# Performance work log

Measured on AMD Instinct MI355X. Metric: run time of the kernel, lower is better.

The kernel has to match this reference:

```python
import jax, jax.numpy as jnp
import numpy as np

N_NODES = 100_000
N_EDGES = 1_600_000
NEG_SLOPE = 0.2

# layer configs: (in_channels, heads, out_channels, has_proj)
LAYERS = [(193, 8, 16, True), (128, 8, 16, False), (128, 8, 16, False), (128, 8, 8, True)]


def _gat_params(key, fin, H, C):
    ks = jax.random.split(key, 6)
    s = 1.0 / np.sqrt(fin)
    Wl = jax.random.normal(ks[0], (fin, H * C), dtype=jnp.float32) * s
    bl = jax.random.normal(ks[1], (H * C,), dtype=jnp.float32) * 0.01
    Wr = jax.random.normal(ks[2], (fin, H * C), dtype=jnp.float32) * s
    br = jax.random.normal(ks[3], (H * C,), dtype=jnp.float32) * 0.01
    att = jax.random.normal(ks[4], (H, C), dtype=jnp.float32) * (1.0 / np.sqrt(C))
    bias = jax.random.normal(ks[5], (H * C,), dtype=jnp.float32) * 0.01
    return Wl, bl, Wr, br, att, bias


def setup_inputs() -> dict:
    key = jax.random.key(0)
    ks = jax.random.split(key, 16)
    inp = {}
    inp['x'] = jax.random.normal(ks[0], (N_NODES, 193), dtype=jnp.float32)
    inp['edge_index'] = jax.random.randint(ks[1], (2, N_EDGES), 0, N_NODES, dtype=jnp.int64)
    for li, (fin, H, C, _) in enumerate(LAYERS, start=1):
        Wl, bl, Wr, br, att, bias = _gat_params(ks[1 + li], fin, H, C)
        inp[f'Wl{li}'] = Wl; inp[f'bl{li}'] = bl
        inp[f'Wr{li}'] = Wr; inp[f'br{li}'] = br
        inp[f'att{li}'] = att; inp[f'bias{li}'] = bias
    # residual projections where in_channels != heads*out_channels
    inp['proj1_W'] = jax.random.normal(ks[8], (193, 128), dtype=jnp.float32) * (1.0 / np.sqrt(193))
    inp['proj1_b'] = jax.random.normal(ks[9], (128,), dtype=jnp.float32) * 0.01
    inp['proj4_W'] = jax.random.normal(ks[10], (128, 64), dtype=jnp.float32) * (1.0 / np.sqrt(128))
    inp['proj4_b'] = jax.random.normal(ks[11], (64,), dtype=jnp.float32) * 0.01
    inp['lin1_W'] = jax.random.normal(ks[12], (64, 32), dtype=jnp.float32) * (1.0 / np.sqrt(64))
    inp['lin1_b'] = jax.random.normal(ks[13], (32,), dtype=jnp.float32) * 0.01
    return inp


def _gatv2(x, src, dst, Wl, bl, Wr, br, att, bias):
    # x: [N, Fin]; att: [H, C]
    N = x.shape[0]
    H, C = att.shape
    xl = (x @ Wl + bl).reshape(N, H, C)  # source transform
    xr = (x @ Wr + br).reshape(N, H, C)  # destination transform
    m = xl[src] + xr[dst]                # [E, H, C] edge gather
    e = jnp.einsum('ehc,hc->eh', jax.nn.leaky_relu(m, NEG_SLOPE), att)  # [E, H]
    emax = jax.ops.segment_max(e, dst, num_segments=N)  # per-dst softmax max
    p = jnp.exp(e - emax[dst])
    denom = jax.ops.segment_sum(p, dst, num_segments=N)
    alpha = p / (denom[dst] + 1e-16)     # [E, H]
    out = jax.ops.segment_sum(alpha[:, :, None] * xl[src], dst, num_segments=N)  # [N, H, C]
    return out.reshape(N, H * C) + bias


def _forward(x, edge_index, params):
    src, dst = edge_index[0], edge_index[1]
    h = x
    for li in range(4):
        Wl, bl, Wr, br, att, bias, projW, projb = params[li]
        g = _gatv2(h, src, dst, Wl, bl, Wr, br, att, bias)
        res = h @ projW + projb if projW is not None else h
        h = jax.nn.gelu(g + res, approximate=False)
    Wf, bf = params[4]
    return h @ Wf + bf


def reference(x, edge_index,
              Wl1, bl1, Wr1, br1, att1, bias1,
              Wl2, bl2, Wr2, br2, att2, bias2,
              Wl3, bl3, Wr3, br3, att3, bias3,
              Wl4, bl4, Wr4, br4, att4, bias4,
              proj1_W, proj1_b, proj4_W, proj4_b, lin1_W, lin1_b):
    params = [
        (Wl1, bl1, Wr1, br1, att1, bias1, proj1_W, proj1_b),
        (Wl2, bl2, Wr2, br2, att2, bias2, None, None),
        (Wl3, bl3, Wr3, br3, att3, bias3, None, None),
        (Wl4, bl4, Wr4, br4, att4, bias4, proj4_W, proj4_b),
        (lin1_W, lin1_b),
    ]
    return _forward(x, edge_index, params)
```

## Files before the change

kernel.cpp:

```cpp
#include <hip/hip_runtime.h>
#include <hip/hip_bf16.h>

#define NNODES 100000
#define NPR 12500
#define SCAP 262144

typedef short s16x8 __attribute__((ext_vector_type(8)));
typedef float f32x4 __attribute__((ext_vector_type(4)));
typedef unsigned long long u64;

__device__ inline ushort f2bf(float f) {
    uint u = __float_as_uint(f);
    uint r = u + 0x7fffu + ((u >> 16) & 1u);
    return (ushort)(r >> 16);
}
__device__ inline float bf2f(ushort u) { return __uint_as_float(((uint)u) << 16); }
__device__ inline float bflo(uint u) { return __uint_as_float(u << 16); }
__device__ inline float bfhi(uint u) { return __uint_as_float(u & 0xffff0000u); }

__device__ inline void gl_lds16(const ushort* g, ushort* l) {
    __builtin_amdgcn_global_load_lds((const __attribute__((address_space(1))) void*)g,
                                     (__attribute__((address_space(3))) void*)l, 16, 0, 0);
}

__global__ void hist_kernel(const int* __restrict__ dst, int E, int* __restrict__ deg) {
    int e = blockIdx.x * blockDim.x + threadIdx.x;
    if (e < E) atomicAdd(&deg[dst[e]], 1);
}

__global__ __launch_bounds__(256) void scan_part(const int* __restrict__ deg,
                                                 int* __restrict__ bsum, int n) {
    int t = threadIdx.x;
    int base = blockIdx.x * 1024 + t * 4;
    int4 v = make_int4(0, 0, 0, 0);
    if (base + 3 < n) v = *(const int4*)(deg + base);
    else {
        if (base + 0 < n) v.x = deg[base + 0];
        if (base + 1 < n) v.y = deg[base + 1];
        if (base + 2 < n) v.z = deg[base + 2];
    }
    int s = v.x + v.y + v.z + v.w;
#pragma unroll
    for (int o = 1; o < 64; o <<= 1) s += __shfl_xor(s, o);
    __shared__ int ws[4];
    if ((t & 63) == 0) ws[t >> 6] = s;
    __syncthreads();
    if (t == 0) bsum[blockIdx.x] = ws[0] + ws[1] + ws[2] + ws[3];
}

__global__ __launch_bounds__(128) void scan_bsum(int* __restrict__ bsum, int nb,
                                                 int* __restrict__ rowptr, int n) {
    __shared__ int s[128];
    int t = threadIdx.x;
    int v = (t < nb) ? bsum[t] : 0;
    s[t] = v;
    __syncthreads();
#pragma unroll
    for (int o = 1; o < 128; o <<= 1) {
        int u = (t >= o) ? s[t - o] : 0;
        __syncthreads();
        s[t] += u;
        __syncthreads();
    }
    if (t < nb) bsum[t] = s[t] - v;
    if (t == 127) rowptr[n] = s[127];
}

__global__ __launch_bounds__(256) void scan_apply(const int* __restrict__ deg,
                                                  const int* __restrict__ bsum,
                                                  int* __restrict__ rowptr, int n) {
    int t = threadIdx.x;
    int base = blockIdx.x * 1024 + t * 4;
    int4 v = make_int4(0, 0, 0, 0);
    if (base + 3 < n) v = *(const int4*)(deg + base);
    else {
        if (base + 0 < n) v.x = deg[base + 0];
        if (base + 1 < n) v.y = deg[base + 1];
        if (base + 2 < n) v.z = deg[base + 2];
    }
    int s = v.x + v.y + v.z + v.w;
    int lane = t & 63, w = t >> 6;
    int incl = s;
#pragma unroll
    for (int o = 1; o < 64; o <<= 1) {
        int u = __shfl_up(incl, o);
        if (lane >= o) incl += u;
    }
    __shared__ int wsum[4];
    if (lane == 63) wsum[w] = incl;
    __syncthreads();
    int woff = 0;
    if (w > 0) woff += wsum[0];
    if (w > 1) woff += wsum[1];
    if (w > 2) woff += wsum[2];
    int off = bsum[blockIdx.x] + woff + (incl - s);
    int4 r;
    r.x = off;
    r.y = off + v.x;
    r.z = r.y + v.y;
    r.w = r.z + v.z;
    if (base + 3 < n) *(int4*)(rowptr + base) = r;
    else {
        if (base + 0 < n) rowptr[base + 0] = r.x;
        if (base + 1 < n) rowptr[base + 1] = r.y;
        if (base + 2 < n) rowptr[base + 2] = r.z;
    }
}

__global__ __launch_bounds__(256) void bucket_edges(const int* __restrict__ src,
                                                    const int* __restrict__ dst, int E,
                                                    int* __restrict__ rcount,
                                                    u64* __restrict__ stage) {
    __shared__ int cnt[8];
    __shared__ int base[8];
    const int t = threadIdx.x;
    if (t < 8) cnt[t] = 0;
    __syncthreads();
    const int e0 = blockIdx.x * 2048 + t;
    int d[8], s[8], r[8], off[8];
#pragma unroll
    for (int i = 0; i < 8; ++i) {
        int e = e0 + i * 256;
        bool v = e < E;
        int ee = min(e, E - 1);
        d[i] = dst[ee];
        s[i] = src[ee];
        r[i] = d[i] / NPR;
        off[i] = v ? atomicAdd(&cnt[r[i]], 1) : -1;
    }
    __syncthreads();
    if (t < 8) base[t] = atomicAdd(&rcount[t], cnt[t]);
    __syncthreads();
#pragma unroll
    for (int i = 0; i < 8; ++i) {
        if (off[i] >= 0) {
            int slot = base[r[i]] + off[i];
            if (slot < SCAP)
                stage[(size_t)r[i] * SCAP + slot] = ((u64)(uint)d[i] << 32) | (uint)s[i];
        }
    }
}

__global__ __launch_bounds__(256) void scatter_ranged(const u64* __restrict__ stage,
                                                      const int* __restrict__ rcount,
                                                      const int* __restrict__ rowptr,
                                                      int* __restrict__ cursor,
                                                      int* __restrict__ csr) {
    const int r = blockIdx.x & 7;
    const int nb = gridDim.x >> 3;
    const int bi = blockIdx.x >> 3;
    const int cnt = min(rcount[r], SCAP);
    const u64* sp = stage + (size_t)r * SCAP;
    for (int i = bi * 256 + threadIdx.x; i < cnt; i += nb * 256) {
        u64 p = sp[i];
        int d = (int)(p >> 32);
        int s = (int)(uint)p;
        int pos = rowptr[d] + atomicAdd(&cursor[d], 1);
        csr[pos] = s;
    }
}

struct WConvDesc { const float* W; ushort* Wt; int K, N, Kp; };
struct WConvArgs { WConvDesc d[10]; };

__global__ void convert_weights(WConvArgs args) {
    WConvDesc dd = args.d[blockIdx.y];
    int total = dd.N * dd.Kp;
    for (int i = blockIdx.x * 256 + threadIdx.x; i < total; i += gridDim.x * 256) {
        int n = i / dd.Kp, k = i - n * dd.Kp;
        float v = (k < dd.K) ? dd.W[(size_t)k * dd.N + n] : 0.f;
        dd.Wt[i] = f2bf(v);
    }
}

struct BCat { const float* src; float* dst; int len; };
struct BCatArgs { BCat d[10]; };
__global__ void concat_bias(BCatArgs a) {
    BCat dd = a.d[blockIdx.x];
    for (int i = threadIdx.x; i < dd.len; i += 256) dd.dst[i] = dd.src[i];
}

__global__ void convert_x(const float* __restrict__ x, ushort* __restrict__ xb, int M) {
    int total = M * 56;
    for (int i = blockIdx.x * 256 + threadIdx.x; i < total; i += gridDim.x * 256) {
        int n = i / 56;
        int k4 = (i - n * 56) * 4;
        ushort o[4];
#pragma unroll
        for (int j = 0; j < 4; ++j) {
            int k = k4 + j;
            o[j] = (k < 193) ? f2bf(x[(size_t)n * 193 + k]) : (ushort)0;
        }
        *(uint2*)(xb + (size_t)n * 224 + k4) = *(const uint2*)o;
    }
}

template <int BN>
__global__ __launch_bounds__(256) void gemm_mfma(const ushort* __restrict__ A,
                                                 const ushort* __restrict__ BtAll,
                                                 const float* __restrict__ biasAll,
                                                 ushort* __restrict__ C,
                                                 int M, int Kp, int Cstride,
                                                 int GX, int NPAN) {
    const int id = blockIdx.x;
    const int xcd = id & 7;
    const int j = id >> 3;
    const int y = j % NPAN;
    const int xblk = (j / NPAN) * 8 + xcd;
    if (xblk >= GX) return;
    const int r0 = xblk * 128;
    const int col0 = y * BN;
    const ushort* Bt = BtAll + (size_t)col0 * Kp;
    const float* bias = biasAll + col0;

    __shared__ ushort As[128 * 32];
    __shared__ ushort Bs[BN * 32];
    const int t = threadIdx.x;
    const int lane = t & 63;
    const int w = t >> 6;
    const int la = lane & 15;
    const int lk = (lane >> 4) * 8;

    constexpr int MR = (BN == 128) ? 4 : 2;
    const int m0 = (BN == 128) ? (w >> 1) * 64 : w * 32;
    const int n0 = (BN == 128) ? (w & 1) * 64 : 0;

    f32x4 acc[MR][4];
#pragma unroll
    for (int i = 0; i < MR; ++i)
#pragma unroll
        for (int j2 = 0; j2 < 4; ++j2) acc[i][j2] = (f32x4)0.f;

    const int lrow4 = lane >> 2;
    const int lkq = (lane & 3) * 8;
    const int arow0 = min(r0 + (2 * w) * 16 + lrow4, M - 1);
    const int arow1 = min(r0 + (2 * w + 1) * 16 + lrow4, M - 1);
    const size_t aoff0 = (size_t)arow0 * Kp + lkq;
    const size_t aoff1 = (size_t)arow1 * Kp + lkq;
    const int brow0 = (BN == 128) ? (2 * w) * 16 + lrow4 : w * 16 + lrow4;
    const int brow1 = (2 * w + 1) * 16 + lrow4;
    const size_t boff0 = (size_t)brow0 * Kp + lkq;
    const size_t boff1 = (size_t)brow1 * Kp + lkq;

    for (int k0 = 0; k0 < Kp; k0 += 32) {
        gl_lds16(A + aoff0 + k0, &As[(2 * w) * 512]);
        gl_lds16(A + aoff1 + k0, &As[(2 * w + 1) * 512]);
        if (BN == 128) {
            gl_lds16(Bt + boff0 + k0, &Bs[(2 * w) * 512]);
            gl_lds16(Bt + boff1 + k0, &Bs[(2 * w + 1) * 512]);
        } else {
            gl_lds16(Bt + boff0 + k0, &Bs[w * 512]);
        }
        asm volatile("s_waitcnt vmcnt(0)" ::: "memory");
        __syncthreads();
        s16x8 av[MR], bv[4];
#pragma unroll
        for (int i = 0; i < MR; ++i)
            av[i] = *(const s16x8*)&As[(m0 + i * 16 + la) * 32 + lk];
#pragma unroll
        for (int j2 = 0; j2 < 4; ++j2)
            bv[j2] = *(const s16x8*)&Bs[(n0 + j2 * 16 + la) * 32 + lk];
#pragma unroll
        for (int i = 0; i < MR; ++i)
#pragma unroll
            for (int j2 = 0; j2 < 4; ++j2)
                acc[i][j2] = __builtin_amdgcn_mfma_f32_16x16x32_bf16(av[i], bv[j2], acc[i][j2], 0, 0, 0);
        __syncthreads();
    }
    const int lrow = (lane >> 4) * 4;
#pragma unroll
    for (int i = 0; i < MR; ++i) {
#pragma unroll
        for (int j2 = 0; j2 < 4; ++j2) {
            int col = n0 + j2 * 16 + la;
            float bval = bias[col];
#pragma unroll
            for (int r = 0; r < 4; ++r) {
                int row = r0 + m0 + i * 16 + lrow + r;
                if (row < M) C[(size_t)row * Cstride + col0 + col] = f2bf(acc[i][j2][r] + bval);
            }
        }
    }
}

__global__ __launch_bounds__(256) void gat_agg128(const ushort* __restrict__ xcat, int xstride,
                                                  int xr_off,
                                                  const ushort* __restrict__ res, int rstride, int roff,
                                                  const float* __restrict__ att,
                                                  const float* __restrict__ bias,
                                                  const int* __restrict__ rowptr,
                                                  const int* __restrict__ csr,
                                                  ushort* __restrict__ houtb, int M) {
    const int n = blockIdx.x * 4 + (threadIdx.x >> 6);
    if (n >= M) return;
    const int lane = threadIdx.x & 63;
    const int clane = lane & 15;
    const int q = lane >> 4;

    const char* xb = (const char*)xcat;
    const uint xrowB = (uint)xstride * 2u;
    const uint chB = (uint)clane * 16u;

    float xr[8], at[8];
    {
        uint4 u = *(const uint4*)(xb + (uint)n * xrowB + (uint)xr_off * 2u + chB);
        xr[0] = bflo(u.x); xr[1] = bfhi(u.x); xr[2] = bflo(u.y); xr[3] = bfhi(u.y);
        xr[4] = bflo(u.z); xr[5] = bfhi(u.z); xr[6] = bflo(u.w); xr[7] = bfhi(u.w);
        const float L2E = 1.4426950408889634f;
        float4 a0 = *(const float4*)(att + 8 * clane);
        float4 a1 = *(const float4*)(att + 8 * clane + 4);
        at[0] = a0.x * L2E; at[1] = a0.y * L2E; at[2] = a0.z * L2E; at[3] = a0.w * L2E;
        at[4] = a1.x * L2E; at[5] = a1.y * L2E; at[6] = a1.z * L2E; at[7] = a1.w * L2E;
    }

    const int s0 = rowptr[n], s1 = rowptr[n + 1];
    float ssum = 0.f;
    float acc[8] = {0.f, 0.f, 0.f, 0.f, 0.f, 0.f, 0.f, 0.f};

    if (s1 > s0) {
        const int nq = (s1 - s0 + 3) >> 2;
        auto ISSUE = [&](uint4& buf, bool& val, int p) {
            if (p >= nq) { val = false; buf = make_uint4(0u, 0u, 0u, 0u); return; }
            int g = s0 + p * 4 + q;
            val = g < s1;
            int src = csr[min(g, s1 - 1)];
            buf = *(const uint4*)(xb + (uint)src * xrowB + chB);
        };
        auto COMPUTE = [&](const uint4& buf, bool val) {
            float x[8];
            x[0] = bflo(buf.x); x[1] = bfhi(buf.x); x[2] = bflo(buf.y); x[3] = bfhi(buf.y);
            x[4] = bflo(buf.z); x[5] = bfhi(buf.z); x[6] = bflo(buf.w); x[7] = bfhi(buf.w);
            float prod = 0.f;
#pragma unroll
            for (int j = 0; j < 8; ++j) {
                float v = x[j] + xr[j];
                float l = fmaxf(v, 0.2f * v);
                prod = fmaf(l, at[j], prod);
            }
            prod += __shfl_xor(prod, 1);
            float pe = val ? exp2f(prod) : 0.f;
            ssum += pe;
#pragma unroll
            for (int j = 0; j < 8; ++j) acc[j] = fmaf(pe, x[j], acc[j]);
        };
        uint4 b0, b1, b2, b3;
        bool v0, v1, v2, v3;
        ISSUE(b0, v0, 0); ISSUE(b1, v1, 1); ISSUE(b2, v2, 2); ISSUE(b3, v3, 3);
        for (int p = 0; p < nq; p += 4) {
            COMPUTE(b0, v0); ISSUE(b0, v0, p + 4);
            if (p + 1 < nq) { COMPUTE(b1, v1); ISSUE(b1, v1, p + 5); }
            if (p + 2 < nq) { COMPUTE(b2, v2); ISSUE(b2, v2, p + 6); }
            if (p + 3 < nq) { COMPUTE(b3, v3); ISSUE(b3, v3, p + 7); }
        }
    }

#pragma unroll
    for (int o = 16; o < 64; o <<= 1) {
        ssum += __shfl_xor(ssum, o);
#pragma unroll
        for (int j = 0; j < 8; ++j) acc[j] += __shfl_xor(acc[j], o);
    }

    float inv = 1.f / (ssum + 1e-16f);
    int ch = 8 * clane + 2 * q;
    float a0s = (q == 0) ? acc[0] : (q == 1) ? acc[2] : (q == 2) ? acc[4] : acc[6];
    float a1s = (q == 0) ? acc[1] : (q == 1) ? acc[3] : (q == 2) ? acc[5] : acc[7];
    uint u = *(const uint*)(res + (size_t)n * rstride + roff + ch);
    float r0v = bflo(u), r1v = bfhi(u);
    float2 b2 = *(const float2*)(bias + ch);
    float y0 = fmaf(a0s, inv, b2.x + r0v);
    float y1 = fmaf(a1s, inv, b2.y + r1v);
    float o0 = 0.5f * y0 * (1.f + erff(y0 * 0.70710678118654752f));
    float o1 = 0.5f * y1 * (1.f + erff(y1 * 0.70710678118654752f));
    *(uint*)(houtb + (size_t)n * 128 + ch) = (uint)f2bf(o0) | ((uint)f2bf(o1) << 16);
}

__global__ __launch_bounds__(256) void gat_agg64_lin(const ushort* __restrict__ xcat, int xstride,
                                                     int xr_off,
                                                     const ushort* __restrict__ res, int rstride, int roff,
                                                     const float* __restrict__ att,
                                                     const float* __restrict__ bias,
                                                     const int* __restrict__ rowptr,
                                                     const int* __restrict__ csr,
                                                     const float* __restrict__ linW,
                                                     const float* __restrict__ linb,
                                                     float* __restrict__ out, int M) {
    __shared__ float Ws[64 * 32];
    __shared__ float hs[4][64];
    {
        int t = threadIdx.x;
#pragma unroll
        for (int i = 0; i < 8; ++i) Ws[t + 256 * i] = linW[t + 256 * i];
    }
    __syncthreads();

    const int wid = threadIdx.x >> 6;
    const int n = blockIdx.x * 4 + wid;
    if (n >= M) return;
    const int lane = threadIdx.x & 63;
    const int clane = lane & 7;
    const int q = lane >> 3;

    const char* xb = (const char*)xcat;
    const uint xrowB = (uint)xstride * 2u;
    const uint chB = (uint)clane * 16u;

    float xr[8], at[8];
    {
        uint4 u = *(const uint4*)(xb + (uint)n * xrowB + (uint)xr_off * 2u + chB);
        xr[0] = bflo(u.x); xr[1] = bfhi(u.x); xr[2] = bflo(u.y); xr[3] = bfhi(u.y);
        xr[4] = bflo(u.z); xr[5] = bfhi(u.z); xr[6] = bflo(u.w); xr[7] = bfhi(u.w);
        const float L2E = 1.4426950408889634f;
        float4 a0 = *(const float4*)(att + 8 * clane);
        float4 a1 = *(const float4*)(att + 8 * clane + 4);
        at[0] = a0.x * L2E; at[1] = a0.y * L2E; at[2] = a0.z * L2E; at[3] = a0.w * L2E;
        at[4] = a1.x * L2E; at[5] = a1.y * L2E; at[6] = a1.z * L2E; at[7] = a1.w * L2E;
    }

    const int s0 = rowptr[n], s1 = rowptr[n + 1];
    float ssum = 0.f;
    float acc[8] = {0.f, 0.f, 0.f, 0.f, 0.f, 0.f, 0.f, 0.f};

    if (s1 > s0) {
        const int nq = (s1 - s0 + 7) >> 3;
        auto ISSUE = [&](uint4& buf, bool& val, int p) {
            if (p >= nq) { val = false; buf = make_uint4(0u, 0u, 0u, 0u); return; }
            int g = s0 + p * 8 + q;
            val = g < s1;
            int src = csr[min(g, s1 - 1)];
            buf = *(const uint4*)(xb + (uint)src * xrowB + chB);
        };
        auto COMPUTE = [&](const uint4& buf, bool val) {
            float x[8];
            x[0] = bflo(buf.x); x[1] = bfhi(buf.x); x[2] = bflo(buf.y); x[3] = bfhi(buf.y);
            x[4] = bflo(buf.z); x[5] = bfhi(buf.z); x[6] = bflo(buf.w); x[7] = bfhi(buf.w);
            float prod = 0.f;
#pragma unroll
            for (int j = 0; j < 8; ++j) {
                float v = x[j] + xr[j];
                float l = fmaxf(v, 0.2f * v);
                prod = fmaf(l, at[j], prod);
            }
            float pe = val ? exp2f(prod) : 0.f;
            ssum += pe;
#pragma unroll
            for (int j = 0; j < 8; ++j) acc[j] = fmaf(pe, x[j], acc[j]);
        };
        uint4 b0, b1, b2, b3;
        bool v0, v1, v2, v3;
        ISSUE(b0, v0, 0); ISSUE(b1, v1, 1); ISSUE(b2, v2, 2); ISSUE(b3, v3, 3);
        for (int p = 0; p < nq; p += 4) {
            COMPUTE(b0, v0); ISSUE(b0, v0, p + 4);
            if (p + 1 < nq) { COMPUTE(b1, v1); ISSUE(b1, v1, p + 5); }
            if (p + 2 < nq) { COMPUTE(b2, v2); ISSUE(b2, v2, p + 6); }
            if (p + 3 < nq) { COMPUTE(b3, v3); ISSUE(b3, v3, p + 7); }
        }
    }

#pragma unroll
    for (int o = 8; o < 64; o <<= 1) {
        ssum += __shfl_xor(ssum, o);
#pragma unroll
        for (int j = 0; j < 8; ++j) acc[j] += __shfl_xor(acc[j], o);
    }

    float inv = 1.f / (ssum + 1e-16f);
    int ch = 8 * clane + q;
    float a0s = (q == 0) ? acc[0] : (q == 1) ? acc[1] : (q == 2) ? acc[2] : (q == 3) ? acc[3]
              : (q == 4) ? acc[4] : (q == 5) ? acc[5] : (q == 6) ? acc[6] : acc[7];
    float r0v = bf2f(res[(size_t)n * rstride + roff + ch]);
    float y0 = fmaf(a0s, inv, bias[ch] + r0v);
    float o0 = 0.5f * y0 * (1.f + erff(y0 * 0.70710678118654752f));

    hs[wid][ch] = o0;
    asm volatile("s_waitcnt lgkmcnt(0)" ::: "memory");
    const int col = lane & 31;
    const int half = lane >> 5;
    const float* hp = &hs[wid][half * 32];
    const float* wp = &Ws[(half * 32) * 32 + col];
    float a = 0.f;
#pragma unroll
    for (int k = 0; k < 32; ++k) a = fmaf(hp[k], wp[k * 32], a);
    a += __shfl_xor(a, 32);
    if (half == 0) out[(size_t)n * 32 + col] = a + linb[col];
}

extern "C" void kernel_launch(void* const* d_in, const int* in_sizes, int n_in,
                              void* d_out, int out_size, void* d_ws, size_t ws_size,
                              hipStream_t stream) {
    const float* x = (const float*)d_in[0];
    const int* ei = (const int*)d_in[1];
    const int E = in_sizes[1] / 2;
    const int* srcp = ei;
    const int* dstp = ei + E;

    const float* Wl[4]  = {(const float*)d_in[2],  (const float*)d_in[8],  (const float*)d_in[14], (const float*)d_in[20]};
    const float* bl[4]  = {(const float*)d_in[3],  (const float*)d_in[9],  (const float*)d_in[15], (const float*)d_in[21]};
    const float* Wr[4]  = {(const float*)d_in[4],  (const float*)d_in[10], (const float*)d_in[16], (const float*)d_in[22]};
    const float* br[4]  = {(const float*)d_in[5],  (const float*)d_in[11], (const float*)d_in[17], (const float*)d_in[23]};
    const float* att[4] = {(const float*)d_in[6],  (const float*)d_in[12], (const float*)d_in[18], (const float*)d_in[24]};
    const float* bia[4] = {(const float*)d_in[7],  (const float*)d_in[13], (const float*)d_in[19], (const float*)d_in[25]};
    const float* proj1W = (const float*)d_in[26];
    const float* proj1b = (const float*)d_in[27];
    const float* proj4W = (const float*)d_in[28];
    const float* proj4b = (const float*)d_in[29];
    const float* linW   = (const float*)d_in[30];
    const float* linb   = (const float*)d_in[31];

    const int M = NNODES;
    ushort* xcat = (ushort*)d_ws;
    ushort* xb   = xcat + (size_t)M * 384;
    ushort* hb1  = xb;
    ushort* hb2  = xb + (size_t)M * 224;
    ushort* wb = hb2 + (size_t)M * 128;
    ushort* WtC1 = wb; wb += 384 * 224;
    ushort* WtC2 = wb; wb += 256 * 128;
    ushort* WtC3 = wb; wb += 256 * 128;
    ushort* WtC4 = wb; wb += 192 * 128;
    float* bc1 = (float*)wb;
    float* bc2 = bc1 + 384;
    float* bc3 = bc2 + 256;
    float* bc4 = bc3 + 256;
    int* deg    = (int*)(bc4 + 192);
    int* cursor = deg + M;
    int* rcount = cursor + M;
    int* rowptr = rcount + 8;
    int* csr    = rowptr + (M + 1);
    int* bsum   = csr + E;
    u64* stage  = (u64*)(((uintptr_t)(bsum + 128) + 7) & ~(uintptr_t)7);

    const int NB = (M + 1023) / 1024;

    hipMemsetAsync(deg, 0, (2 * (size_t)M + 8) * sizeof(int), stream);
    hist_kernel<<<(E + 255) / 256, 256, 0, stream>>>(dstp, E, deg);
    scan_part<<<NB, 256, 0, stream>>>(deg, bsum, M);
    scan_bsum<<<1, 128, 0, stream>>>(bsum, NB, rowptr, M);
    scan_apply<<<NB, 256, 0, stream>>>(deg, bsum, rowptr, M);
    bucket_edges<<<(E + 2047) / 2048, 256, 0, stream>>>(srcp, dstp, E, rcount, stage);
    scatter_ranged<<<8 * 96, 256, 0, stream>>>(stage, rcount, rowptr, cursor, csr);

    WConvArgs wa;
    wa.d[0] = {Wl[0],  WtC1,             193, 128, 224};
    wa.d[1] = {Wr[0],  WtC1 + 128 * 224, 193, 128, 224};
    wa.d[2] = {proj1W, WtC1 + 256 * 224, 193, 128, 224};
    wa.d[3] = {Wl[1],  WtC2,             128, 128, 128};
    wa.d[4] = {Wr[1],  WtC2 + 128 * 128, 128, 128, 128};
    wa.d[5] = {Wl[2],  WtC3,             128, 128, 128};
    wa.d[6] = {Wr[2],  WtC3 + 128 * 128, 128, 128, 128};
    wa.d[7] = {Wl[3],  WtC4,             128, 64, 128};
    wa.d[8] = {Wr[3],  WtC4 + 64 * 128,  128, 64, 128};
    wa.d[9] = {proj4W, WtC4 + 128 * 128, 128, 64, 128};
    convert_weights<<<dim3(112, 10), 256, 0, stream>>>(wa);
    BCatArgs ba;
    ba.d[0] = {bl[0],  bc1,       128};
    ba.d[1] = {br[0],  bc1 + 128, 128};
    ba.d[2] = {proj1b, bc1 + 256, 128};
    ba.d[3] = {bl[1],  bc2,       128};
    ba.d[4] = {br[1],  bc2 + 128, 128};
    ba.d[5] = {bl[2],  bc3,       128};
    ba.d[6] = {br[2],  bc3 + 128, 128};
    ba.d[7] = {bl[3],  bc4,       64};
    ba.d[8] = {br[3],  bc4 + 64,  64};
    ba.d[9] = {proj4b, bc4 + 128, 64};
    concat_bias<<<10, 256, 0, stream>>>(ba);
    convert_x<<<2048, 256, 0, stream>>>(x, xb, M);

    const int GX = (M + 127) / 128;
    const int S8 = ((GX + 7) / 8) * 8;
    dim3 ag((M + 3) / 4, 1);

    gemm_mfma<128><<<S8 * 3, 256, 0, stream>>>(xb, WtC1, bc1, xcat, M, 224, 384, GX, 3);
    gat_agg128<<<ag, 256, 0, stream>>>(xcat, 384, 128, xcat, 384, 256, att[0], bia[0],
                                       rowptr, csr, hb1, M);
    gemm_mfma<128><<<S8 * 2, 256, 0, stream>>>(hb1, WtC2, bc2, xcat, M, 128, 256, GX, 2);
    gat_agg128<<<ag, 256, 0, stream>>>(xcat, 256, 128, hb1, 128, 0, att[1], bia[1],
                                       rowptr, csr, hb2, M);
    gemm_mfma<128><<<S8 * 2, 256, 0, stream>>>(hb2, WtC3, bc3, xcat, M, 128, 256, GX, 2);
    gat_agg128<<<ag, 256, 0, stream>>>(xcat, 256, 128, hb2, 128, 0, att[2], bia[2],
                                       rowptr, csr, hb1, M);
    gemm_mfma<64><<<S8 * 3, 256, 0, stream>>>(hb1, WtC4, bc4, xcat, M, 128, 192, GX, 3);
    gat_agg64_lin<<<ag, 256, 0, stream>>>(xcat, 192, 64, xcat, 192, 128, att[3], bia[3],
                                          rowptr, csr, linW, linb, (float*)d_out, M);
}
```

Before: 639.8 us.

## Fuse x conversion into first GEMM, double-buffer GEMM tiles, reorder CSR build

Removes the separate fp32-to-bf16 conversion of x by adding a GEMM variant that reads fp32 rows directly and converts them while staging into LDS. The existing bf16 GEMM gets double-buffered LDS tiles with partial vmcnt waits, so the next tile's loads overlap the MFMA work. The degree histogram now runs over dst-bucketed staging data after bucket_edges, which localizes the atomics, and the weight conversion and bias concat kernels are merged into one launch. In exchange the fp32 A loads are uncoalesced scalar reads with bounds checks, and LDS use rises.

```diff
diff --git a/kernel.cpp b/kernel.cpp
--- a/kernel.cpp
+++ b/kernel.cpp
@@ -23,9 +23,50 @@
                                      (__attribute__((address_space(3))) void*)l, 16, 0, 0);
 }
 
-__global__ void hist_kernel(const int* __restrict__ dst, int E, int* __restrict__ deg) {
-    int e = blockIdx.x * blockDim.x + threadIdx.x;
-    if (e < E) atomicAdd(&deg[dst[e]], 1);
+__global__ __launch_bounds__(256) void bucket_edges(const int* __restrict__ src,
+                                                    const int* __restrict__ dst, int E,
+                                                    int* __restrict__ rcount,
+                                                    u64* __restrict__ stage) {
+    __shared__ int cnt[8];
+    __shared__ int base[8];
+    const int t = threadIdx.x;
+    if (t < 8) cnt[t] = 0;
+    __syncthreads();
+    const int e0 = blockIdx.x * 2048 + t;
+    int d[8], s[8], r[8], off[8];
+#pragma unroll
+    for (int i = 0; i < 8; ++i) {
+        int e = e0 + i * 256;
+        bool v = e < E;
+        int ee = min(e, E - 1);
+        d[i] = dst[ee];
+        s[i] = src[ee];
+        r[i] = d[i] / NPR;
+        off[i] = v ? atomicAdd(&cnt[r[i]], 1) : -1;
+    }
+    __syncthreads();
+    if (t < 8) base[t] = atomicAdd(&rcount[t], cnt[t]);
+    __syncthreads();
+#pragma unroll
+    for (int i = 0; i < 8; ++i) {
+        if (off[i] >= 0) {
+            int slot = base[r[i]] + off[i];
+            if (slot < SCAP)
+                stage[(size_t)r[i] * SCAP + slot] = ((u64)(uint)d[i] << 32) | (uint)s[i];
+        }
+    }
+}
+
+__global__ __launch_bounds__(256) void hist_ranged(const u64* __restrict__ stage,
+                                                   const int* __restrict__ rcount,
+                                                   int* __restrict__ deg) {
+    const int r = blockIdx.x & 7;
+    const int nb = gridDim.x >> 3;
+    const int bi = blockIdx.x >> 3;
+    const int cnt = min(rcount[r], SCAP);
+    const u64* sp = stage + (size_t)r * SCAP;
+    for (int i = bi * 256 + threadIdx.x; i < cnt; i += nb * 256)
+        atomicAdd(&deg[(int)(sp[i] >> 32)], 1);
 }
 
 __global__ __launch_bounds__(256) void scan_part(const int* __restrict__ deg,
@@ -107,40 +148,6 @@
     }
 }
 
-__global__ __launch_bounds__(256) void bucket_edges(const int* __restrict__ src,
-                                                    const int* __restrict__ dst, int E,
-                                                    int* __restrict__ rcount,
-                                                    u64* __restrict__ stage) {
-    __shared__ int cnt[8];
-    __shared__ int base[8];
-    const int t = threadIdx.x;
-    if (t < 8) cnt[t] = 0;
-    __syncthreads();
-    const int e0 = blockIdx.x * 2048 + t;
-    int d[8], s[8], r[8], off[8];
-#pragma unroll
-    for (int i = 0; i < 8; ++i) {
-        int e = e0 + i * 256;
-        bool v = e < E;
-        int ee = min(e, E - 1);
-        d[i] = dst[ee];
-        s[i] = src[ee];
-        r[i] = d[i] / NPR;
-        off[i] = v ? atomicAdd(&cnt[r[i]], 1) : -1;
-    }
-    __syncthreads();
-    if (t < 8) base[t] = atomicAdd(&rcount[t], cnt[t]);
-    __syncthreads();
-#pragma unroll
-    for (int i = 0; i < 8; ++i) {
-        if (off[i] >= 0) {
-            int slot = base[r[i]] + off[i];
-            if (slot < SCAP)
-                stage[(size_t)r[i] * SCAP + slot] = ((u64)(uint)d[i] << 32) | (uint)s[i];
-        }
-    }
-}
-
 __global__ __launch_bounds__(256) void scatter_ranged(const u64* __restrict__ stage,
                                                       const int* __restrict__ rcount,
                                                       const int* __restrict__ rowptr,
@@ -161,37 +168,131 @@
 }
 
 struct WConvDesc { const float* W; ushort* Wt; int K, N, Kp; };
-struct WConvArgs { WConvDesc d[10]; };
-
-__global__ void convert_weights(WConvArgs args) {
-    WConvDesc dd = args.d[blockIdx.y];
-    int total = dd.N * dd.Kp;
-    for (int i = blockIdx.x * 256 + threadIdx.x; i < total; i += gridDim.x * 256) {
-        int n = i / dd.Kp, k = i - n * dd.Kp;
-        float v = (k < dd.K) ? dd.W[(size_t)k * dd.N + n] : 0.f;
-        dd.Wt[i] = f2bf(v);
-    }
-}
-
 struct BCat { const float* src; float* dst; int len; };
-struct BCatArgs { BCat d[10]; };
-__global__ void concat_bias(BCatArgs a) {
-    BCat dd = a.d[blockIdx.x];
-    for (int i = threadIdx.x; i < dd.len; i += 256) dd.dst[i] = dd.src[i];
-}
-
-__global__ void convert_x(const float* __restrict__ x, ushort* __restrict__ xb, int M) {
-    int total = M * 56;
-    for (int i = blockIdx.x * 256 + threadIdx.x; i < total; i += gridDim.x * 256) {
-        int n = i / 56;
-        int k4 = (i - n * 56) * 4;
-        ushort o[4];
+struct ConvArgs { WConvDesc d[10]; BCat b[10]; };
+
+__global__ void convert_wb(ConvArgs args) {
+    if (blockIdx.y < 10) {
+        WConvDesc dd = args.d[blockIdx.y];
+        int total = dd.N * dd.Kp;
+        for (int i = blockIdx.x * 256 + threadIdx.x; i < total; i += gridDim.x * 256) {
+            int n = i / dd.Kp, k = i - n * dd.Kp;
+            float v = (k < dd.K) ? dd.W[(size_t)k * dd.N + n] : 0.f;
+            dd.Wt[i] = f2bf(v);
+        }
+    } else if (blockIdx.x < 10) {
+        BCat bb = args.b[blockIdx.x];
+        for (int i = threadIdx.x; i < bb.len; i += 256) bb.dst[i] = bb.src[i];
+    }
+}
+
+__global__ __launch_bounds__(256) void gemm_mfma_f32(const float* __restrict__ A,
+                                                     const ushort* __restrict__ BtAll,
+                                                     const float* __restrict__ biasAll,
+                                                     ushort* __restrict__ C,
+                                                     int M, int Cstride, int GX, int NPAN) {
+    constexpr int KF = 193, NT = 7;
+    const int id = blockIdx.x;
+    const int xcd = id & 7;
+    const int jj = id >> 3;
+    const int y = jj % NPAN;
+    const int xblk = (jj / NPAN) * 8 + xcd;
+    if (xblk >= GX) return;
+    const int r0 = xblk * 128;
+    const int col0 = y * 128;
+    const ushort* Bt = BtAll + (size_t)col0 * 224;
+    const float* bias = biasAll + col0;
+
+    __shared__ ushort As[128 * 32];
+    __shared__ ushort Bs[2][128 * 32];
+    const int t = threadIdx.x;
+    const int lane = t & 63;
+    const int w = t >> 6;
+    const int la = lane & 15;
+    const int lk = (lane >> 4) * 8;
+    const int m0 = (w >> 1) * 64;
+    const int n0 = (w & 1) * 64;
+
+    f32x4 acc[4][4];
+#pragma unroll
+    for (int i = 0; i < 4; ++i)
+#pragma unroll
+        for (int j = 0; j < 4; ++j) acc[i][j] = (f32x4)0.f;
+
+    const int arow = t >> 3;
+    const int fq = t & 7;
+    const float* Ap[4];
+#pragma unroll
+    for (int p = 0; p < 4; ++p)
+        Ap[p] = A + (size_t)min(r0 + p * 32 + arow, M - 1) * KF + fq * 4;
+
+    const int lrow4 = lane >> 2;
+    const int lkq = (lane & 3) * 8;
+    const size_t boff0 = (size_t)((2 * w) * 16 + lrow4) * 224 + lkq;
+    const size_t boff1 = (size_t)((2 * w + 1) * 16 + lrow4) * 224 + lkq;
+
+    float ra[16], rn[16];
+    auto LOADA = [&](float* r, int k0) {
+#pragma unroll
+        for (int p = 0; p < 4; ++p)
+#pragma unroll
+            for (int j = 0; j < 4; ++j) {
+                int k = k0 + fq * 4 + j;
+                r[p * 4 + j] = (k < KF) ? Ap[p][k0 + j] : 0.f;
+            }
+    };
+    auto STAGEB = [&](int b, int k0) {
+        gl_lds16(Bt + boff0 + k0, &Bs[b][(2 * w) * 512]);
+        gl_lds16(Bt + boff1 + k0, &Bs[b][(2 * w + 1) * 512]);
+    };
+    auto WRITEA = [&](const float* r) {
+#pragma unroll
+        for (int p = 0; p < 4; ++p) {
+            uint2 pk;
+            pk.x = (uint)f2bf(r[p * 4 + 0]) | ((uint)f2bf(r[p * 4 + 1]) << 16);
+            pk.y = (uint)f2bf(r[p * 4 + 2]) | ((uint)f2bf(r[p * 4 + 3]) << 16);
+            *(uint2*)&As[(p * 32 + arow) * 32 + fq * 4] = pk;
+        }
+    };
+
+    STAGEB(0, 0);
+    LOADA(ra, 0);
+    int cur = 0;
+#pragma unroll
+    for (int tt = 0; tt < NT; ++tt) {
+        if (tt + 1 < NT) { STAGEB(cur ^ 1, (tt + 1) * 32); LOADA(rn, (tt + 1) * 32); }
+        WRITEA(ra);
+        __syncthreads();
+        s16x8 av[4], bv[4];
+#pragma unroll
+        for (int i = 0; i < 4; ++i)
+            av[i] = *(const s16x8*)&As[(m0 + i * 16 + la) * 32 + lk];
+#pragma unroll
+        for (int j = 0; j < 4; ++j)
+            bv[j] = *(const s16x8*)&Bs[cur][(n0 + j * 16 + la) * 32 + lk];
+#pragma unroll
+        for (int i = 0; i < 4; ++i)
+#pragma unroll
+            for (int j = 0; j < 4; ++j)
+                acc[i][j] = __builtin_amdgcn_mfma_f32_16x16x32_bf16(av[i], bv[j], acc[i][j], 0, 0, 0);
+        __syncthreads();
+#pragma unroll
+        for (int q2 = 0; q2 < 16; ++q2) ra[q2] = rn[q2];
+        cur ^= 1;
+    }
+    const int lrow = (lane >> 4) * 4;
+#pragma unroll
+    for (int i = 0; i < 4; ++i) {
 #pragma unroll
         for (int j = 0; j < 4; ++j) {
-            int k = k4 + j;
-            o[j] = (k < 193) ? f2bf(x[(size_t)n * 193 + k]) : (ushort)0;
-        }
-        *(uint2*)(xb + (size_t)n * 224 + k4) = *(const uint2*)o;
+            int col = n0 + j * 16 + la;
+            float bval = bias[col];
+#pragma unroll
+            for (int r = 0; r < 4; ++r) {
+                int row = r0 + m0 + i * 16 + lrow + r;
+                if (row < M) C[(size_t)row * Cstride + col0 + col] = f2bf(acc[i][j][r] + bval);
+            }
+        }
     }
 }
 
@@ -204,17 +305,17 @@
                                                  int GX, int NPAN) {
     const int id = blockIdx.x;
     const int xcd = id & 7;
-    const int j = id >> 3;
-    const int y = j % NPAN;
-    const int xblk = (j / NPAN) * 8 + xcd;
+    const int jj = id >> 3;
+    const int y = jj % NPAN;
+    const int xblk = (jj / NPAN) * 8 + xcd;
     if (xblk >= GX) return;
     const int r0 = xblk * 128;
     const int col0 = y * BN;
     const ushort* Bt = BtAll + (size_t)col0 * Kp;
     const float* bias = biasAll + col0;
 
-    __shared__ ushort As[128 * 32];
-    __shared__ ushort Bs[BN * 32];
+    __shared__ ushort As[2][128 * 32];
+    __shared__ ushort Bs[2][BN * 32];
     const int t = threadIdx.x;
     const int lane = t & 63;
     const int w = t >> 6;
@@ -242,30 +343,43 @@
     const size_t boff0 = (size_t)brow0 * Kp + lkq;
     const size_t boff1 = (size_t)brow1 * Kp + lkq;
 
-    for (int k0 = 0; k0 < Kp; k0 += 32) {
-        gl_lds16(A + aoff0 + k0, &As[(2 * w) * 512]);
-        gl_lds16(A + aoff1 + k0, &As[(2 * w + 1) * 512]);
+    auto STAGE = [&](int b, int k0) {
+        gl_lds16(A + aoff0 + k0, &As[b][(2 * w) * 512]);
+        gl_lds16(A + aoff1 + k0, &As[b][(2 * w + 1) * 512]);
         if (BN == 128) {
-            gl_lds16(Bt + boff0 + k0, &Bs[(2 * w) * 512]);
-            gl_lds16(Bt + boff1 + k0, &Bs[(2 * w + 1) * 512]);
+            gl_lds16(Bt + boff0 + k0, &Bs[b][(2 * w) * 512]);
+            gl_lds16(Bt + boff1 + k0, &Bs[b][(2 * w + 1) * 512]);
         } else {
-            gl_lds16(Bt + boff0 + k0, &Bs[w * 512]);
-        }
-        asm volatile("s_waitcnt vmcnt(0)" ::: "memory");
+            gl_lds16(Bt + boff0 + k0, &Bs[b][w * 512]);
+        }
+    };
+
+    const int NT = Kp >> 5;
+    STAGE(0, 0);
+    int cur = 0;
+    for (int tt = 0; tt < NT; ++tt) {
+        if (tt + 1 < NT) {
+            STAGE(cur ^ 1, (tt + 1) * 32);
+            if (BN == 128) asm volatile("s_waitcnt vmcnt(4)" ::: "memory");
+            else           asm volatile("s_waitcnt vmcnt(3)" ::: "memory");
+        } else {
+            asm volatile("s_waitcnt vmcnt(0)" ::: "memory");
+        }
         __syncthreads();
         s16x8 av[MR], bv[4];
 #pragma unroll
         for (int i = 0; i < MR; ++i)
-            av[i] = *(const s16x8*)&As[(m0 + i * 16 + la) * 32 + lk];
+            av[i] = *(const s16x8*)&As[cur][(m0 + i * 16 + la) * 32 + lk];
 #pragma unroll
         for (int j2 = 0; j2 < 4; ++j2)
-            bv[j2] = *(const s16x8*)&Bs[(n0 + j2 * 16 + la) * 32 + lk];
+            bv[j2] = *(const s16x8*)&Bs[cur][(n0 + j2 * 16 + la) * 32 + lk];
 #pragma unroll
         for (int i = 0; i < MR; ++i)
 #pragma unroll
             for (int j2 = 0; j2 < 4; ++j2)
                 acc[i][j2] = __builtin_amdgcn_mfma_f32_16x16x32_bf16(av[i], bv[j2], acc[i][j2], 0, 0, 0);
         __syncthreads();
+        cur ^= 1;
     }
     const int lrow = (lane >> 4) * 4;
 #pragma unroll
@@ -509,9 +623,8 @@
 
     const int M = NNODES;
     ushort* xcat = (ushort*)d_ws;
-    ushort* xb   = xcat + (size_t)M * 384;
-    ushort* hb1  = xb;
-    ushort* hb2  = xb + (size_t)M * 224;
+    ushort* hb1  = xcat + (size_t)M * 384;
+    ushort* hb2  = hb1 + (size_t)M * 128;
     ushort* wb = hb2 + (size_t)M * 128;
     ushort* WtC1 = wb; wb += 384 * 224;
     ushort* WtC2 = wb; wb += 256 * 128;
@@ -532,44 +645,41 @@
     const int NB = (M + 1023) / 1024;
 
     hipMemsetAsync(deg, 0, (2 * (size_t)M + 8) * sizeof(int), stream);
-    hist_kernel<<<(E + 255) / 256, 256, 0, stream>>>(dstp, E, deg);
+    bucket_edges<<<(E + 2047) / 2048, 256, 0, stream>>>(srcp, dstp, E, rcount, stage);
+    hist_ranged<<<8 * 96, 256, 0, stream>>>(stage, rcount, deg);
     scan_part<<<NB, 256, 0, stream>>>(deg, bsum, M);
     scan_bsum<<<1, 128, 0, stream>>>(bsum, NB, rowptr, M);
     scan_apply<<<NB, 256, 0, stream>>>(deg, bsum, rowptr, M);
-    bucket_edges<<<(E + 2047) / 2048, 256, 0, stream>>>(srcp, dstp, E, rcount, stage);
     scatter_ranged<<<8 * 96, 256, 0, stream>>>(stage, rcount, rowptr, cursor, csr);
 
-    WConvArgs wa;
-    wa.d[0] = {Wl[0],  WtC1,             193, 128, 224};
-    wa.d[1] = {Wr[0],  WtC1 + 128 * 224, 193, 128, 224};
-    wa.d[2] = {proj1W, WtC1 + 256 * 224, 193, 128, 224};
-    wa.d[3] = {Wl[1],  WtC2,             128, 128, 128};
-    wa.d[4] = {Wr[1],  WtC2 + 128 * 128, 128, 128, 128};
-    wa.d[5] = {Wl[2],  WtC3,             128, 128, 128};
-    wa.d[6] = {Wr[2],  WtC3 + 128 * 128, 128, 128, 128};
-    wa.d[7] = {Wl[3],  WtC4,             128, 64, 128};
-    wa.d[8] = {Wr[3],  WtC4 + 64 * 128,  128, 64, 128};
-    wa.d[9] = {proj4W, WtC4 + 128 * 128, 128, 64, 128};
-    convert_weights<<<dim3(112, 10), 256, 0, stream>>>(wa);
-    BCatArgs ba;
-    ba.d[0] = {bl[0],  bc1,       128};
-    ba.d[1] = {br[0],  bc1 + 128, 128};
-    ba.d[2] = {proj1b, bc1 + 256, 128};
-    ba.d[3] = {bl[1],  bc2,       128};
-    ba.d[4] = {br[1],  bc2 + 128, 128};
-    ba.d[5] = {bl[2],  bc3,       128};
-    ba.d[6] = {br[2],  bc3 + 128, 128};
-    ba.d[7] = {bl[3],  bc4,       64};
-    ba.d[8] = {br[3],  bc4 + 64,  64};
-    ba.d[9] = {proj4b, bc4 + 128, 64};
-    concat_bias<<<10, 256, 0, stream>>>(ba);
-    convert_x<<<2048, 256, 0, stream>>>(x, xb, M);
+    ConvArgs ca;
+    ca.d[0] = {Wl[0],  WtC1,             193, 128, 224};
+    ca.d[1] = {Wr[0],  WtC1 + 128 * 224, 193, 128, 224};
+    ca.d[2] = {proj1W, WtC1 + 256 * 224, 193, 128, 224};
+    ca.d[3] = {Wl[1],  WtC2,             128, 128, 128};
+    ca.d[4] = {Wr[1],  WtC2 + 128 * 128, 128, 128, 128};
+    ca.d[5] = {Wl[2],  WtC3,             128, 128, 128};
+    ca.d[6] = {Wr[2],  WtC3 + 128 * 128, 128, 128, 128};
+    ca.d[7] = {Wl[3],  WtC4,             128, 64, 128};
+    ca.d[8] = {Wr[3],  WtC4 + 64 * 128,  128, 64, 128};
+    ca.d[9] = {proj4W, WtC4 + 128 * 128, 128, 64, 128};
+    ca.b[0] = {bl[0],  bc1,       128};
+    ca.b[1] = {br[0],  bc1 + 128, 128};
+    ca.b[2] = {proj1b, bc1 + 256, 128};
+    ca.b[3] = {bl[1],  bc2,       128};
+    ca.b[4] = {br[1],  bc2 + 128, 128};
+    ca.b[5] = {bl[2],  bc3,       128};
+    ca.b[6] = {br[2],  bc3 + 128, 128};
+    ca.b[7] = {bl[3],  bc4,       64};
+    ca.b[8] = {br[3],  bc4 + 64,  64};
+    ca.b[9] = {proj4b, bc4 + 128, 64};
+    convert_wb<<<dim3(112, 11), 256, 0, stream>>>(ca);
 
     const int GX = (M + 127) / 128;
     const int S8 = ((GX + 7) / 8) * 8;
     dim3 ag((M + 3) / 4, 1);
 
-    gemm_mfma<128><<<S8 * 3, 256, 0, stream>>>(xb, WtC1, bc1, xcat, M, 224, 384, GX, 3);
+    gemm_mfma_f32<<<S8 * 3, 256, 0, stream>>>(x, WtC1, bc1, xcat, M, 384, GX, 3);
     gat_agg128<<<ag, 256, 0, stream>>>(xcat, 384, 128, xcat, 384, 256, att[0], bia[0],
                                        rowptr, csr, hb1, M);
     gemm_mfma<128><<<S8 * 2, 256, 0, stream>>>(hb1, WtC2, bc2, xcat, M, 128, 256, GX, 2);
```

Measured after the change: 641.4 us. Within noise of the previous version (+0.2%).

## Double-buffer GEMM LDS tiles, histogram from bucketed stage, merge weight/bias conversion

Applied to the files above, without the earlier changes.

The GEMM now double-buffers its A/B LDS tiles and issues the next K-slice's global-to-LDS loads before waiting on the current one, so load latency overlaps with MFMA work. The degree histogram is computed from the range-bucketed staging buffer instead of raw dst, which gives more localized atomics. The weight conversion and bias concat launches are merged into one kernel to save a launch. The cost is double the LDS per GEMM block, which may reduce occupancy.

```diff
diff --git a/kernel.cpp b/kernel.cpp
--- a/kernel.cpp
+++ b/kernel.cpp
@@ -23,9 +23,50 @@
                                      (__attribute__((address_space(3))) void*)l, 16, 0, 0);
 }
 
-__global__ void hist_kernel(const int* __restrict__ dst, int E, int* __restrict__ deg) {
-    int e = blockIdx.x * blockDim.x + threadIdx.x;
-    if (e < E) atomicAdd(&deg[dst[e]], 1);
+__global__ __launch_bounds__(256) void bucket_edges(const int* __restrict__ src,
+                                                    const int* __restrict__ dst, int E,
+                                                    int* __restrict__ rcount,
+                                                    u64* __restrict__ stage) {
+    __shared__ int cnt[8];
+    __shared__ int base[8];
+    const int t = threadIdx.x;
+    if (t < 8) cnt[t] = 0;
+    __syncthreads();
+    const int e0 = blockIdx.x * 2048 + t;
+    int d[8], s[8], r[8], off[8];
+#pragma unroll
+    for (int i = 0; i < 8; ++i) {
+        int e = e0 + i * 256;
+        bool v = e < E;
+        int ee = min(e, E - 1);
+        d[i] = dst[ee];
+        s[i] = src[ee];
+        r[i] = d[i] / NPR;
+        off[i] = v ? atomicAdd(&cnt[r[i]], 1) : -1;
+    }
+    __syncthreads();
+    if (t < 8) base[t] = atomicAdd(&rcount[t], cnt[t]);
+    __syncthreads();
+#pragma unroll
+    for (int i = 0; i < 8; ++i) {
+        if (off[i] >= 0) {
+            int slot = base[r[i]] + off[i];
+            if (slot < SCAP)
+                stage[(size_t)r[i] * SCAP + slot] = ((u64)(uint)d[i] << 32) | (uint)s[i];
+        }
+    }
+}
+
+__global__ __launch_bounds__(256) void hist_ranged(const u64* __restrict__ stage,
+                                                   const int* __restrict__ rcount,
+                                                   int* __restrict__ deg) {
+    const int r = blockIdx.x & 7;
+    const int nb = gridDim.x >> 3;
+    const int bi = blockIdx.x >> 3;
+    const int cnt = min(rcount[r], SCAP);
+    const u64* sp = stage + (size_t)r * SCAP;
+    for (int i = bi * 256 + threadIdx.x; i < cnt; i += nb * 256)
+        atomicAdd(&deg[(int)(sp[i] >> 32)], 1);
 }
 
 __global__ __launch_bounds__(256) void scan_part(const int* __restrict__ deg,
@@ -107,40 +148,6 @@
     }
 }
 
-__global__ __launch_bounds__(256) void bucket_edges(const int* __restrict__ src,
-                                                    const int* __restrict__ dst, int E,
-                                                    int* __restrict__ rcount,
-                                                    u64* __restrict__ stage) {
-    __shared__ int cnt[8];
-    __shared__ int base[8];
-    const int t = threadIdx.x;
-    if (t < 8) cnt[t] = 0;
-    __syncthreads();
-    const int e0 = blockIdx.x * 2048 + t;
-    int d[8], s[8], r[8], off[8];
-#pragma unroll
-    for (int i = 0; i < 8; ++i) {
-        int e = e0 + i * 256;
-        bool v = e < E;
-        int ee = min(e, E - 1);
-        d[i] = dst[ee];
-        s[i] = src[ee];
-        r[i] = d[i] / NPR;
-        off[i] = v ? atomicAdd(&cnt[r[i]], 1) : -1;
-    }
-    __syncthreads();
-    if (t < 8) base[t] = atomicAdd(&rcount[t], cnt[t]);
-    __syncthreads();
-#pragma unroll
-    for (int i = 0; i < 8; ++i) {
-        if (off[i] >= 0) {
-            int slot = base[r[i]] + off[i];
-            if (slot < SCAP)
-                stage[(size_t)r[i] * SCAP + slot] = ((u64)(uint)d[i] << 32) | (uint)s[i];
-        }
-    }
-}
-
 __global__ __launch_bounds__(256) void scatter_ranged(const u64* __restrict__ stage,
                                                       const int* __restrict__ rcount,
                                                       const int* __restrict__ rowptr,
@@ -161,23 +168,22 @@
 }
 
 struct WConvDesc { const float* W; ushort* Wt; int K, N, Kp; };
-struct WConvArgs { WConvDesc d[10]; };
-
-__global__ void convert_weights(WConvArgs args) {
-    WConvDesc dd = args.d[blockIdx.y];
-    int total = dd.N * dd.Kp;
-    for (int i = blockIdx.x * 256 + threadIdx.x; i < total; i += gridDim.x * 256) {
-        int n = i / dd.Kp, k = i - n * dd.Kp;
-        float v = (k < dd.K) ? dd.W[(size_t)k * dd.N + n] : 0.f;
-        dd.Wt[i] = f2bf(v);
-    }
-}
-
 struct BCat { const float* src; float* dst; int len; };
-struct BCatArgs { BCat d[10]; };
-__global__ void concat_bias(BCatArgs a) {
-    BCat dd = a.d[blockIdx.x];
-    for (int i = threadIdx.x; i < dd.len; i += 256) dd.dst[i] = dd.src[i];
+struct ConvArgs { WConvDesc d[10]; BCat b[10]; };
+
+__global__ void convert_wb(ConvArgs args) {
+    if (blockIdx.y < 10) {
+        WConvDesc dd = args.d[blockIdx.y];
+        int total = dd.N * dd.Kp;
+        for (int i = blockIdx.x * 256 + threadIdx.x; i < total; i += gridDim.x * 256) {
+            int n = i / dd.Kp, k = i - n * dd.Kp;
+            float v = (k < dd.K) ? dd.W[(size_t)k * dd.N + n] : 0.f;
+            dd.Wt[i] = f2bf(v);
+        }
+    } else if (blockIdx.x < 10) {
+        BCat bb = args.b[blockIdx.x];
+        for (int i = threadIdx.x; i < bb.len; i += 256) bb.dst[i] = bb.src[i];
+    }
 }
 
 __global__ void convert_x(const float* __restrict__ x, ushort* __restrict__ xb, int M) {
@@ -204,17 +210,17 @@
                                                  int GX, int NPAN) {
     const int id = blockIdx.x;
     const int xcd = id & 7;
-    const int j = id >> 3;
-    const int y = j % NPAN;
-    const int xblk = (j / NPAN) * 8 + xcd;
+    const int jj = id >> 3;
+    const int y = jj % NPAN;
+    const int xblk = (jj / NPAN) * 8 + xcd;
     if (xblk >= GX) return;
     const int r0 = xblk * 128;
     const int col0 = y * BN;
     const ushort* Bt = BtAll + (size_t)col0 * Kp;
     const float* bias = biasAll + col0;
 
-    __shared__ ushort As[128 * 32];
-    __shared__ ushort Bs[BN * 32];
+    __shared__ ushort As[2][128 * 32];
+    __shared__ ushort Bs[2][BN * 32];
     const int t = threadIdx.x;
     const int lane = t & 63;
     const int w = t >> 6;
@@ -242,30 +248,43 @@
     const size_t boff0 = (size_t)brow0 * Kp + lkq;
     const size_t boff1 = (size_t)brow1 * Kp + lkq;
 
-    for (int k0 = 0; k0 < Kp; k0 += 32) {
-        gl_lds16(A + aoff0 + k0, &As[(2 * w) * 512]);
-        gl_lds16(A + aoff1 + k0, &As[(2 * w + 1) * 512]);
+    auto STAGE = [&](int b, int k0) {
+        gl_lds16(A + aoff0 + k0, &As[b][(2 * w) * 512]);
+        gl_lds16(A + aoff1 + k0, &As[b][(2 * w + 1) * 512]);
         if (BN == 128) {
-            gl_lds16(Bt + boff0 + k0, &Bs[(2 * w) * 512]);
-            gl_lds16(Bt + boff1 + k0, &Bs[(2 * w + 1) * 512]);
+            gl_lds16(Bt + boff0 + k0, &Bs[b][(2 * w) * 512]);
+            gl_lds16(Bt + boff1 + k0, &Bs[b][(2 * w + 1) * 512]);
         } else {
-            gl_lds16(Bt + boff0 + k0, &Bs[w * 512]);
-        }
-        asm volatile("s_waitcnt vmcnt(0)" ::: "memory");
+            gl_lds16(Bt + boff0 + k0, &Bs[b][w * 512]);
+        }
+    };
+
+    const int NT = Kp >> 5;
+    STAGE(0, 0);
+    int cur = 0;
+    for (int tt = 0; tt < NT; ++tt) {
+        if (tt + 1 < NT) {
+            STAGE(cur ^ 1, (tt + 1) * 32);
+            if (BN == 128) asm volatile("s_waitcnt vmcnt(4)" ::: "memory");
+            else           asm volatile("s_waitcnt vmcnt(3)" ::: "memory");
+        } else {
+            asm volatile("s_waitcnt vmcnt(0)" ::: "memory");
+        }
         __syncthreads();
         s16x8 av[MR], bv[4];
 #pragma unroll
         for (int i = 0; i < MR; ++i)
-            av[i] = *(const s16x8*)&As[(m0 + i * 16 + la) * 32 + lk];
+            av[i] = *(const s16x8*)&As[cur][(m0 + i * 16 + la) * 32 + lk];
 #pragma unroll
         for (int j2 = 0; j2 < 4; ++j2)
-            bv[j2] = *(const s16x8*)&Bs[(n0 + j2 * 16 + la) * 32 + lk];
+            bv[j2] = *(const s16x8*)&Bs[cur][(n0 + j2 * 16 + la) * 32 + lk];
 #pragma unroll
         for (int i = 0; i < MR; ++i)
 #pragma unroll
             for (int j2 = 0; j2 < 4; ++j2)
                 acc[i][j2] = __builtin_amdgcn_mfma_f32_16x16x32_bf16(av[i], bv[j2], acc[i][j2], 0, 0, 0);
         __syncthreads();
+        cur ^= 1;
     }
     const int lrow = (lane >> 4) * 4;
 #pragma unroll
@@ -532,37 +551,35 @@
     const int NB = (M + 1023) / 1024;
 
     hipMemsetAsync(deg, 0, (2 * (size_t)M + 8) * sizeof(int), stream);
-    hist_kernel<<<(E + 255) / 256, 256, 0, stream>>>(dstp, E, deg);
+    bucket_edges<<<(E + 2047) / 2048, 256, 0, stream>>>(srcp, dstp, E, rcount, stage);
+    hist_ranged<<<8 * 96, 256, 0, stream>>>(stage, rcount, deg);
     scan_part<<<NB, 256, 0, stream>>>(deg, bsum, M);
     scan_bsum<<<1, 128, 0, stream>>>(bsum, NB, rowptr, M);
     scan_apply<<<NB, 256, 0, stream>>>(deg, bsum, rowptr, M);
-    bucket_edges<<<(E + 2047) / 2048, 256, 0, stream>>>(srcp, dstp, E, rcount, stage);
     scatter_ranged<<<8 * 96, 256, 0, stream>>>(stage, rcount, rowptr, cursor, csr);
 
-    WConvArgs wa;
-    wa.d[0] = {Wl[0],  WtC1,             193, 128, 224};
-    wa.d[1] = {Wr[0],  WtC1 + 128 * 224, 193, 128, 224};
-    wa.d[2] = {proj1W, WtC1 + 256 * 224, 193, 128, 224};
-    wa.d[3] = {Wl[1],  WtC2,             128, 128, 128};
-    wa.d[4] = {Wr[1],  WtC2 + 128 * 128, 128, 128, 128};
-    wa.d[5] = {Wl[2],  WtC3,             128, 128, 128};
-    wa.d[6] = {Wr[2],  WtC3 + 128 * 128, 128, 128, 128};
-    wa.d[7] = {Wl[3],  WtC4,             128, 64, 128};
-    wa.d[8] = {Wr[3],  WtC4 + 64 * 128,  128, 64, 128};
-    wa.d[9] = {proj4W, WtC4 + 128 * 128, 128, 64, 128};
-    convert_weights<<<dim3(112, 10), 256, 0, stream>>>(wa);
-    BCatArgs ba;
-    ba.d[0] = {bl[0],  bc1,       128};
-    ba.d[1] = {br[0],  bc1 + 128, 128};
-    ba.d[2] = {proj1b, bc1 + 256, 128};
-    ba.d[3] = {bl[1],  bc2,       128};
-    ba.d[4] = {br[1],  bc2 + 128, 128};
-    ba.d[5] = {bl[2],  bc3,       128};
-    ba.d[6] = {br[2],  bc3 + 128, 128};
-    ba.d[7] = {bl[3],  bc4,       64};
-    ba.d[8] = {br[3],  bc4 + 64,  64};
-    ba.d[9] = {proj4b, bc4 + 128, 64};
-    concat_bias<<<10, 256, 0, stream>>>(ba);
+    ConvArgs ca;
+    ca.d[0] = {Wl[0],  WtC1,             193, 128, 224};
+    ca.d[1] = {Wr[0],  WtC1 + 128 * 224, 193, 128, 224};
+    ca.d[2] = {proj1W, WtC1 + 256 * 224, 193, 128, 224};
+    ca.d[3] = {Wl[1],  WtC2,             128, 128, 128};
+    ca.d[4] = {Wr[1],  WtC2 + 128 * 128, 128, 128, 128};
+    ca.d[5] = {Wl[2],  WtC3,             128, 128, 128};
+    ca.d[6] = {Wr[2],  WtC3 + 128 * 128, 128, 128, 128};
+    ca.d[7] = {Wl[3],  WtC4,             128, 64, 128};
+    ca.d[8] = {Wr[3],  WtC4 + 64 * 128,  128, 64, 128};
+    ca.d[9] = {proj4W, WtC4 + 128 * 128, 128, 64, 128};
+    ca.b[0] = {bl[0],  bc1,       128};
+    ca.b[1] = {br[0],  bc1 + 128, 128};
+    ca.b[2] = {proj1b, bc1 + 256, 128};
+    ca.b[3] = {bl[1],  bc2,       128};
+    ca.b[4] = {br[1],  bc2 + 128, 128};
+    ca.b[5] = {bl[2],  bc3,       128};
+    ca.b[6] = {br[2],  bc3 + 128, 128};
+    ca.b[7] = {bl[3],  bc4,       64};
+    ca.b[8] = {br[3],  bc4 + 64,  64};
+    ca.b[9] = {proj4b, bc4 + 128, 64};
+    convert_wb<<<dim3(112, 11), 256, 0, stream>>>(ca);
     convert_x<<<2048, 256, 0, stream>>>(x, xb, M);
 
     const int GX = (M + 127) / 128;
```

New measurement: 662.4 us. 3.5% more time.
